# Kernel optimization log

Measured on AMD Instinct MI355X. Metric: run time of the kernel, lower is better.

## Reference

```python
import jax, jax.numpy as jnp
import numpy as np

B, D, N, K, T = 8192, 256, 2048, 512, 8
M_MARGIN = 1.0
LAMBDA_ORTHO = 1e-3
EPS = 1e-10


def _l2(a, b):
    # squared L2 distance along last axis
    return jnp.sum((a - b) ** 2, axis=-1)


def setup_inputs() -> dict:
    key = jax.random.key(0)
    k1, k2, k3, k4, k5 = jax.random.split(key, 5)
    return {
        "v": jax.random.normal(k1, (B, D), dtype=jnp.float32),
        "vhat": jax.random.normal(k2, (B, D), dtype=jnp.float32),
        "g": jax.random.uniform(k3, (B, K), dtype=jnp.float32),
        "F": jax.random.normal(k4, (K, D), dtype=jnp.float32),
        "negatives": jax.random.normal(k5, (N, D), dtype=jnp.float32),
        "mask": jnp.ones((B,), dtype=bool),
    }


def reference(v, vhat, g, F, negatives, mask):
    maskf = mask.astype(v.dtype)
    msum = maskf.sum()

    # ---- contrastive loss (vectorized over the N-negatives loop) ----
    true_dist = _l2(vhat, v)                                   # [B]
    neg_dist = _l2(vhat[:, None, :], negatives[None, :, :])    # [B, N]
    per = jnp.maximum(1.0 + true_dist[:, None] - neg_dist, 0.0)
    ju_per = per.mean(axis=1) * maskf                          # [B]
    Ju = jnp.where(msum == 0, 0.0, ju_per.sum() / msum)

    # ---- focal triplet loss (topk smallest g, gather F rows) ----
    _, idx = jax.lax.top_k(-g, T)                              # [B, T] indices of t smallest
    g_tz = jnp.take_along_axis(g, idx, axis=1)                 # [B, T]
    F_t = F[idx]                                               # [B, T, D]
    g_t = g_tz / (g_tz.sum(axis=1, keepdims=True) + EPS)
    m_t = M_MARGIN * (1.0 - g_t) ** 2                          # [B, T]
    d_neg = _l2(vhat[:, None, :], F_t)                         # [B, T]
    cur = jnp.maximum(m_t + true_dist[:, None] - d_neg, 0.0)
    jt_per = cur.sum(axis=1) * maskf
    Jt = jnp.where(msum == 0, 0.0, jt_per.sum() / msum)

    # ---- orthogonality regularizer: ||F F^T - I||_F, then squared ----
    gram = F @ F.T - jnp.eye(K, dtype=F.dtype)
    ortho = jnp.sqrt(jnp.sum(gram ** 2))

    Jz = Ju + Jt + LAMBDA_ORTHO * ortho ** 2
    return Jz
```

## Files before the change

### kernel.cpp

```cpp
#include <hip/hip_runtime.h>

#define B_N 8192
#define D_N 256
#define N_N 2048
#define K_N 512
#define T_N 8

using short8  = __attribute__((ext_vector_type(8))) short;
using floatx4 = __attribute__((ext_vector_type(4))) float;


__device__ __forceinline__ float wave_reduce_sum(float x) {
  #pragma unroll
  for (int off = 32; off > 0; off >>= 1) x += __shfl_down(x, off, 64);
  return x;
}

__device__ __forceinline__ unsigned int f2bf(float x) {
  unsigned u = __float_as_uint(x);
  return (u + 0x7fffu + ((u >> 16) & 1u)) >> 16;
}

__device__ __forceinline__ unsigned int pack2bf(float x, float y) {
  return f2bf(x) | (f2bf(y) << 16);
}

__device__ __forceinline__ void gload16(const unsigned short* g, unsigned short* l) {
  __builtin_amdgcn_global_load_lds(
      (const __attribute__((address_space(1))) unsigned int*)g,
      (__attribute__((address_space(3))) unsigned int*)l, 16, 0, 0);
}

__global__ __launch_bounds__(256) void prep_kernel(
    const float* __restrict__ v, const float* __restrict__ vhat,
    const float* __restrict__ neg, const float* __restrict__ F,
    unsigned short* __restrict__ vhat_bf, unsigned short* __restrict__ neg_bf,
    unsigned short* __restrict__ F_bf,
    float* __restrict__ td, float* __restrict__ vn2, float* __restrict__ cb,
    float* __restrict__ nn2, float* __restrict__ fn2) {
  int lane = threadIdx.x & 63;
  int row = (blockIdx.x << 2) + (threadIdx.x >> 6);
  if (row < B_N) {
    const float4 a = *(const float4*)(vhat + (size_t)row * D_N + lane * 4);
    const float4 b = *(const float4*)(v + (size_t)row * D_N + lane * 4);
    float dx = a.x - b.x, dy = a.y - b.y, dz = a.z - b.z, dw = a.w - b.w;
    float t = dx * dx + dy * dy + dz * dz + dw * dw;
    float n = a.x * a.x + a.y * a.y + a.z * a.z + a.w * a.w;
    uint2 p;
    p.x = pack2bf(a.x, a.y);
    p.y = pack2bf(a.z, a.w);
    *(uint2*)(vhat_bf + (size_t)row * D_N + lane * 4) = p;
    t = wave_reduce_sum(t);
    n = wave_reduce_sum(n);
    if (lane == 0) {
      td[row] = t;
      vn2[row] = n;
      cb[row] = 1.0f + t - n;
    }
  } else if (row < B_N + N_N) {
    int r = row - B_N;
    const float4 a = *(const float4*)(neg + (size_t)r * D_N + lane * 4);
    float n = a.x * a.x + a.y * a.y + a.z * a.z + a.w * a.w;
    uint2 p;
    p.x = pack2bf(a.x, a.y);
    p.y = pack2bf(a.z, a.w);
    *(uint2*)(neg_bf + (size_t)r * D_N + lane * 4) = p;
    n = wave_reduce_sum(n);
    if (lane == 0) nn2[r] = n;
  } else {
    int r = row - (B_N + N_N);
    const float4 a = *(const float4*)(F + (size_t)r * D_N + lane * 4);
    float n = a.x * a.x + a.y * a.y + a.z * a.z + a.w * a.w;
    uint2 p;
    p.x = pack2bf(a.x, a.y);
    p.y = pack2bf(a.z, a.w);
    *(uint2*)(F_bf + (size_t)r * D_N + lane * 4) = p;
    n = wave_reduce_sum(n);
    if (lane == 0) fn2[r] = n;
  }
}

__global__ __launch_bounds__(256) void main_kernel(
    const unsigned short* __restrict__ vhat_bf, const unsigned short* __restrict__ neg_bf,
    const unsigned short* __restrict__ F_bf,
    const float* __restrict__ g, const float* __restrict__ F,
    const float* __restrict__ vhat_f,
    const float* __restrict__ td, const float* __restrict__ vn2,
    const float* __restrict__ cb, const float* __restrict__ nn2,
    const float* __restrict__ fn2, const int* __restrict__ mask,
    float* __restrict__ ju_part, float* __restrict__ jt_row,
    float* __restrict__ or_part) {
  __shared__ __align__(16) unsigned char smem[16384];
  const int bx = blockIdx.x;
  const int tid = threadIdx.x;
  const int lane = tid & 63;
  const int wave = tid >> 6;

  if (bx < 1040) {
    const bool is_ju = bx < 1024;
    unsigned short* AsU = (unsigned short*)smem;
    unsigned short* BsU = AsU + 4096;
    int r0, c0;
    const unsigned short *Abase, *Bbase;
    if (is_ju) {
      r0 = (bx >> 4) * 128;
      c0 = (bx & 15) * 128;
      Abase = vhat_bf;
      Bbase = neg_bf;
    } else {
      int o = bx - 1024;
      r0 = (o >> 2) * 128;
      c0 = (o & 3) * 128;
      Abase = F_bf;
      Bbase = F_bf;
    }
    const int wx = wave & 1, wy = wave >> 1;

    const int c_slot = lane & 3;
    const int rA0 = wave * 32 + (lane >> 2);
    const int rA1 = rA0 + 16;
    const int cg0 = c_slot ^ ((rA0 >> 1) & 3);
    const int cg1 = c_slot ^ ((rA1 >> 1) & 3);
    const unsigned short* gA0 = Abase + (size_t)(r0 + rA0) * D_N + cg0 * 8;
    const unsigned short* gA1 = Abase + (size_t)(r0 + rA1) * D_N + cg1 * 8;
    const unsigned short* gB0 = Bbase + (size_t)(c0 + rA0) * D_N + cg0 * 8;
    const unsigned short* gB1 = Bbase + (size_t)(c0 + rA1) * D_N + cg1 * 8;
    unsigned short* lA0 = AsU + wave * 1024 + lane * 8;
    unsigned short* lA1 = lA0 + 512;
    unsigned short* lB0 = BsU + wave * 1024 + lane * 8;
    unsigned short* lB1 = lB0 + 512;

    const int fr = lane & 15;
    const int fc = lane >> 4;
    int aoff[4], boff[4];
    #pragma unroll
    for (int i = 0; i < 4; ++i) {
      int ra = wy * 64 + i * 16 + fr;
      aoff[i] = ra * 32 + (fc ^ ((ra >> 1) & 3)) * 8;
      int rb = wx * 64 + i * 16 + fr;
      boff[i] = rb * 32 + (fc ^ ((rb >> 1) & 3)) * 8;
    }

    floatx4 acc[4][4];
    #pragma unroll
    for (int i = 0; i < 4; ++i)
      #pragma unroll
      for (int j = 0; j < 4; ++j)
        acc[i][j] = floatx4{0.0f, 0.0f, 0.0f, 0.0f};

    for (int k0 = 0; k0 < D_N; k0 += 32) {
      __syncthreads();
      gload16(gA0 + k0, lA0);
      gload16(gA1 + k0, lA1);
      gload16(gB0 + k0, lB0);
      gload16(gB1 + k0, lB1);
      __syncthreads();
      short8 af[4], bf[4];
      #pragma unroll
      for (int i = 0; i < 4; ++i) af[i] = *(const short8*)(AsU + aoff[i]);
      #pragma unroll
      for (int j = 0; j < 4; ++j) bf[j] = *(const short8*)(BsU + boff[j]);
      #pragma unroll
      for (int i = 0; i < 4; ++i)
        #pragma unroll
        for (int j = 0; j < 4; ++j)
          acc[i][j] = __builtin_amdgcn_mfma_f32_16x16x32_bf16(af[i], bf[j], acc[i][j], 0, 0, 0);
    }

    if (is_ju) {
      float nns[4];
      #pragma unroll
      for (int j = 0; j < 4; ++j)
        nns[j] = nn2[c0 + wx * 64 + j * 16 + (lane & 15)];
      float lsum = 0.0f;
      #pragma unroll
      for (int i = 0; i < 4; ++i) {
        #pragma unroll
        for (int r = 0; r < 4; ++r) {
          int b = r0 + wy * 64 + i * 16 + (lane >> 4) * 4 + r;
          float cbb = cb[b];
          float mf = (mask[b] != 0) ? 1.0f : 0.0f;
          float rs = 0.0f;
          #pragma unroll
          for (int j = 0; j < 4; ++j) {
            float val = cbb + 2.0f * acc[i][j][r] - nns[j];
            rs += fmaxf(val, 0.0f);
          }
          lsum += mf * rs;
        }
      }
      lsum = wave_reduce_sum(lsum);
      if (lane == 0) ju_part[bx * 4 + wave] = lsum;
    } else {
      float lsum = 0.0f;
      #pragma unroll
      for (int i = 0; i < 4; ++i) {
        #pragma unroll
        for (int r = 0; r < 4; ++r) {
          int gi = r0 + wy * 64 + i * 16 + (lane >> 4) * 4 + r;
          #pragma unroll
          for (int j = 0; j < 4; ++j) {
            int gj = c0 + wx * 64 + j * 16 + (lane & 15);
            float s = (gi == gj) ? (fn2[gi] - 1.0f) : acc[i][j][r];
            lsum += s * s;
          }
        }
      }
      lsum = wave_reduce_sum(lsum);
      if (lane == 0) or_part[(bx - 1024) * 4 + wave] = lsum;
    }

  } else {
    int b = ((bx - 1040) << 2) + wave;
    const float* grow = g + (size_t)b * K_N;
    float gv[8];
    {
      float4 g0 = *(const float4*)(grow + lane * 8);
      float4 g1 = *(const float4*)(grow + lane * 8 + 4);
      gv[0] = g0.x; gv[1] = g0.y; gv[2] = g0.z; gv[3] = g0.w;
      gv[4] = g1.x; gv[5] = g1.y; gv[6] = g1.z; gv[7] = g1.w;
    }
    unsigned used = 0;
    float sel_val[T_N];
    int sel_idx[T_N];
    for (int t = 0; t < T_N; ++t) {
      float lv = 3.0e38f;
      int lj = 0;
      #pragma unroll
      for (int j = 0; j < 8; ++j) {
        bool ok = (((used >> j) & 1u) == 0u) && (gv[j] < lv);
        lv = ok ? gv[j] : lv;
        lj = ok ? j : lj;
      }
      float rv = lv;
      int ri = lane * 8 + lj;
      #pragma unroll
      for (int off = 32; off > 0; off >>= 1) {
        float ov = __shfl_down(rv, off, 64);
        int oi = __shfl_down(ri, off, 64);
        if (ov < rv) { rv = ov; ri = oi; }
      }
      rv = __shfl(rv, 0, 64);
      ri = __shfl(ri, 0, 64);
      if ((ri >> 3) == lane) used |= 1u << (ri & 7);
      sel_val[t] = rv;
      sel_idx[t] = ri;
    }
    float gsum = 1e-10f;
    #pragma unroll
    for (int t = 0; t < T_N; ++t) gsum += sel_val[t];
    float4 vh = *(const float4*)(vhat_f + (size_t)b * D_N + lane * 4);
    float tdb = td[b], vnb = vn2[b];
    float jtb = 0.0f;
    #pragma unroll
    for (int t = 0; t < T_N; ++t) {
      const float* Fr = F + (size_t)sel_idx[t] * D_N;
      float4 f4 = *(const float4*)(Fr + lane * 4);
      float p = vh.x * f4.x + vh.y * f4.y + vh.z * f4.z + vh.w * f4.w;
      p = wave_reduce_sum(p);
      p = __shfl(p, 0, 64);
      float dneg = vnb - 2.0f * p + fn2[sel_idx[t]];
      float gt = sel_val[t] / gsum;
      float mt = (1.0f - gt) * (1.0f - gt);
      float cur = mt + tdb - dneg;
      jtb += cur > 0.0f ? cur : 0.0f;
    }
    if (lane == 0) jt_row[b] = jtb * ((mask[b] != 0) ? 1.0f : 0.0f);
  }
}

__global__ __launch_bounds__(256) void finalize_kernel(
    const float* __restrict__ jt_row, const float* __restrict__ ju_part,
    const float* __restrict__ or_part, const int* __restrict__ mask,
    float* __restrict__ out) {
  int tid = threadIdx.x;
  float sjt = 0.0f, sju = 0.0f, sor = 0.0f, sm = 0.0f;
  for (int i = tid; i < B_N; i += 256) {
    sjt += jt_row[i];
    sm += (mask[i] != 0) ? 1.0f : 0.0f;
  }
  for (int i = tid; i < 4096; i += 256) sju += ju_part[i];
  if (tid < 64) sor = or_part[tid];
  sjt = wave_reduce_sum(sjt);
  sju = wave_reduce_sum(sju);
  sor = wave_reduce_sum(sor);
  sm  = wave_reduce_sum(sm);
  __shared__ float red[4][4];
  int lane = tid & 63, w = tid >> 6;
  if (lane == 0) {
    red[w][0] = sjt; red[w][1] = sju; red[w][2] = sor; red[w][3] = sm;
  }
  __syncthreads();
  if (tid == 0) {
    float jt = red[0][0] + red[1][0] + red[2][0] + red[3][0];
    float ju = red[0][1] + red[1][1] + red[2][1] + red[3][1];
    float oo = red[0][2] + red[1][2] + red[2][2] + red[3][2];
    float ms = red[0][3] + red[1][3] + red[2][3] + red[3][3];
    float Ju = (ms == 0.0f) ? 0.0f : ju / ((float)N_N * ms);
    float Jt = (ms == 0.0f) ? 0.0f : jt / ms;
    out[0] = Ju + Jt + 1.0e-3f * oo;
  }
}

extern "C" void kernel_launch(void* const* d_in, const int* in_sizes, int n_in,
                              void* d_out, int out_size, void* d_ws, size_t ws_size,
                              hipStream_t stream) {
  (void)in_sizes; (void)n_in; (void)out_size; (void)ws_size;
  const float* v    = (const float*)d_in[0];
  const float* vhat = (const float*)d_in[1];
  const float* g    = (const float*)d_in[2];
  const float* F    = (const float*)d_in[3];
  const float* neg  = (const float*)d_in[4];
  const int*   mask = (const int*)d_in[5];

  float* ws = (float*)d_ws;
  float* td      = ws;
  float* vn2     = ws + 8192;
  float* cb      = ws + 16384;
  float* nn2     = ws + 24576;
  float* fn2     = ws + 26624;
  float* jt_row  = ws + 27136;
  float* ju_part = ws + 35328;
  float* or_part = ws + 39424;
  unsigned short* vhat_bf = (unsigned short*)(ws + 39680);
  unsigned short* neg_bf  = vhat_bf + (size_t)B_N * D_N;
  unsigned short* F_bf    = neg_bf + (size_t)N_N * D_N;

  prep_kernel<<<(B_N + N_N + K_N) / 4, 256, 0, stream>>>(
      v, vhat, neg, F, vhat_bf, neg_bf, F_bf, td, vn2, cb, nn2, fn2);
  main_kernel<<<1024 + 16 + 2048, 256, 0, stream>>>(
      vhat_bf, neg_bf, F_bf, g, F, vhat, td, vn2, cb, nn2, fn2, mask,
      ju_part, jt_row, or_part);
  finalize_kernel<<<1, 256, 0, stream>>>(jt_row, ju_part, or_part, mask, (float*)d_out);
}
```

Baseline: 127.8 us.

## Compute triplet dot products via dense vhat·F^T MFMA GEMM and bitonic top-k

```diff
diff --git a/kernel.cpp b/kernel.cpp
--- a/kernel.cpp
+++ b/kernel.cpp
@@ -31,13 +31,26 @@
       (__attribute__((address_space(3))) unsigned int*)l, 16, 0, 0);
 }
 
+#define CSWAP(a, b)                                              \
+  {                                                              \
+    bool sw_ = sv[a] > sv[b];                                    \
+    float tv_ = sw_ ? sv[a] : sv[b];                             \
+    sv[a] = sw_ ? sv[b] : sv[a];                                 \
+    sv[b] = tv_;                                                 \
+    int ti_ = sw_ ? si[a] : si[b];                               \
+    si[a] = sw_ ? si[b] : si[a];                                 \
+    si[b] = ti_;                                                 \
+  }
+
 __global__ __launch_bounds__(256) void prep_kernel(
     const float* __restrict__ v, const float* __restrict__ vhat,
     const float* __restrict__ neg, const float* __restrict__ F,
+    const float* __restrict__ g,
     unsigned short* __restrict__ vhat_bf, unsigned short* __restrict__ neg_bf,
     unsigned short* __restrict__ F_bf,
     float* __restrict__ td, float* __restrict__ vn2, float* __restrict__ cb,
-    float* __restrict__ nn2, float* __restrict__ fn2) {
+    float* __restrict__ nn2, float* __restrict__ fn2,
+    float* __restrict__ selc, int* __restrict__ seli) {
   int lane = threadIdx.x & 63;
   int row = (blockIdx.x << 2) + (threadIdx.x >> 6);
   if (row < B_N) {
@@ -56,6 +69,60 @@
       td[row] = t;
       vn2[row] = n;
       cb[row] = 1.0f + t - n;
+    }
+    const float* grow = g + (size_t)row * K_N;
+    float sv[8];
+    int si[8];
+    {
+      float4 g0 = *(const float4*)(grow + lane * 8);
+      float4 g1 = *(const float4*)(grow + lane * 8 + 4);
+      sv[0] = g0.x; sv[1] = g0.y; sv[2] = g0.z; sv[3] = g0.w;
+      sv[4] = g1.x; sv[5] = g1.y; sv[6] = g1.z; sv[7] = g1.w;
+      #pragma unroll
+      for (int j = 0; j < 8; ++j) si[j] = lane * 8 + j;
+    }
+    CSWAP(0,1) CSWAP(2,3) CSWAP(4,5) CSWAP(6,7)
+    CSWAP(0,2) CSWAP(1,3) CSWAP(4,6) CSWAP(5,7)
+    CSWAP(1,2) CSWAP(5,6)
+    CSWAP(0,4) CSWAP(1,5) CSWAP(2,6) CSWAP(3,7)
+    CSWAP(2,4) CSWAP(3,5)
+    CSWAP(1,2) CSWAP(3,4) CSWAP(5,6)
+    #pragma unroll
+    for (int rr = 0; rr < 6; ++rr) {
+      const int msk = 1 << rr;
+      float pv[8];
+      int pi[8];
+      #pragma unroll
+      for (int j = 0; j < 8; ++j) {
+        pv[j] = __shfl_xor(sv[j], msk, 64);
+        pi[j] = __shfl_xor(si[j], msk, 64);
+      }
+      float cv[8];
+      int ci[8];
+      #pragma unroll
+      for (int j = 0; j < 8; ++j) {
+        bool mine = sv[j] <= pv[7 - j];
+        cv[j] = mine ? sv[j] : pv[7 - j];
+        ci[j] = mine ? si[j] : pi[7 - j];
+      }
+      #pragma unroll
+      for (int j = 0; j < 8; ++j) { sv[j] = cv[j]; si[j] = ci[j]; }
+      CSWAP(0,4) CSWAP(1,5) CSWAP(2,6) CSWAP(3,7)
+      CSWAP(0,2) CSWAP(1,3) CSWAP(4,6) CSWAP(5,7)
+      CSWAP(0,1) CSWAP(2,3) CSWAP(4,5) CSWAP(6,7)
+    }
+    float gsum = 1e-10f;
+    #pragma unroll
+    for (int t8 = 0; t8 < T_N; ++t8) gsum += sv[t8];
+    if (lane == 0) {
+      float base = t - n;
+      #pragma unroll
+      for (int t8 = 0; t8 < T_N; ++t8) {
+        float gt = sv[t8] / gsum;
+        float mt = (1.0f - gt) * (1.0f - gt);
+        selc[(size_t)row * T_N + t8] = mt + base;
+        seli[(size_t)row * T_N + t8] = si[t8];
+      }
     }
   } else if (row < B_N + N_N) {
     int r = row - B_N;
@@ -83,204 +150,190 @@
 __global__ __launch_bounds__(256) void main_kernel(
     const unsigned short* __restrict__ vhat_bf, const unsigned short* __restrict__ neg_bf,
     const unsigned short* __restrict__ F_bf,
-    const float* __restrict__ g, const float* __restrict__ F,
-    const float* __restrict__ vhat_f,
-    const float* __restrict__ td, const float* __restrict__ vn2,
     const float* __restrict__ cb, const float* __restrict__ nn2,
     const float* __restrict__ fn2, const int* __restrict__ mask,
-    float* __restrict__ ju_part, float* __restrict__ jt_row,
-    float* __restrict__ or_part) {
+    float* __restrict__ ju_part, float* __restrict__ or_part,
+    float* __restrict__ W) {
   __shared__ __align__(16) unsigned char smem[16384];
   const int bx = blockIdx.x;
   const int tid = threadIdx.x;
   const int lane = tid & 63;
   const int wave = tid >> 6;
 
-  if (bx < 1040) {
-    const bool is_ju = bx < 1024;
-    unsigned short* AsU = (unsigned short*)smem;
-    unsigned short* BsU = AsU + 4096;
-    int r0, c0;
-    const unsigned short *Abase, *Bbase;
-    if (is_ju) {
-      r0 = (bx >> 4) * 128;
-      c0 = (bx & 15) * 128;
-      Abase = vhat_bf;
-      Bbase = neg_bf;
-    } else {
-      int o = bx - 1024;
-      r0 = (o >> 2) * 128;
-      c0 = (o & 3) * 128;
-      Abase = F_bf;
-      Bbase = F_bf;
-    }
-    const int wx = wave & 1, wy = wave >> 1;
-
-    const int c_slot = lane & 3;
-    const int rA0 = wave * 32 + (lane >> 2);
-    const int rA1 = rA0 + 16;
-    const int cg0 = c_slot ^ ((rA0 >> 1) & 3);
-    const int cg1 = c_slot ^ ((rA1 >> 1) & 3);
-    const unsigned short* gA0 = Abase + (size_t)(r0 + rA0) * D_N + cg0 * 8;
-    const unsigned short* gA1 = Abase + (size_t)(r0 + rA1) * D_N + cg1 * 8;
-    const unsigned short* gB0 = Bbase + (size_t)(c0 + rA0) * D_N + cg0 * 8;
-    const unsigned short* gB1 = Bbase + (size_t)(c0 + rA1) * D_N + cg1 * 8;
-    unsigned short* lA0 = AsU + wave * 1024 + lane * 8;
-    unsigned short* lA1 = lA0 + 512;
-    unsigned short* lB0 = BsU + wave * 1024 + lane * 8;
-    unsigned short* lB1 = lB0 + 512;
-
-    const int fr = lane & 15;
-    const int fc = lane >> 4;
-    int aoff[4], boff[4];
+  unsigned short* AsU = (unsigned short*)smem;
+  unsigned short* BsU = AsU + 4096;
+  int r0, c0;
+  const unsigned short *Abase, *Bbase;
+  int seg;
+  if (bx < 1024) {
+    seg = 0;
+    r0 = (bx >> 4) * 128;
+    c0 = (bx & 15) * 128;
+    Abase = vhat_bf;
+    Bbase = neg_bf;
+  } else if (bx < 1040) {
+    seg = 1;
+    int o = bx - 1024;
+    r0 = (o >> 2) * 128;
+    c0 = (o & 3) * 128;
+    Abase = F_bf;
+    Bbase = F_bf;
+  } else {
+    seg = 2;
+    int o = bx - 1040;
+    r0 = (o >> 2) * 128;
+    c0 = (o & 3) * 128;
+    Abase = vhat_bf;
+    Bbase = F_bf;
+  }
+  const int wx = wave & 1, wy = wave >> 1;
+
+  const int c_slot = lane & 3;
+  const int rA0 = wave * 32 + (lane >> 2);
+  const int rA1 = rA0 + 16;
+  const int cg0 = c_slot ^ ((rA0 >> 1) & 3);
+  const int cg1 = c_slot ^ ((rA1 >> 1) & 3);
+  const unsigned short* gA0 = Abase + (size_t)(r0 + rA0) * D_N + cg0 * 8;
+  const unsigned short* gA1 = Abase + (size_t)(r0 + rA1) * D_N + cg1 * 8;
+  const unsigned short* gB0 = Bbase + (size_t)(c0 + rA0) * D_N + cg0 * 8;
+  const unsigned short* gB1 = Bbase + (size_t)(c0 + rA1) * D_N + cg1 * 8;
+  unsigned short* lA0 = AsU + wave * 1024 + lane * 8;
+  unsigned short* lA1 = lA0 + 512;
+  unsigned short* lB0 = BsU + wave * 1024 + lane * 8;
+  unsigned short* lB1 = lB0 + 512;
+
+  const int fr = lane & 15;
+  const int fc = lane >> 4;
+  int aoff[4], boff[4];
+  #pragma unroll
+  for (int i = 0; i < 4; ++i) {
+    int ra = wy * 64 + i * 16 + fr;
+    aoff[i] = ra * 32 + (fc ^ ((ra >> 1) & 3)) * 8;
+    int rb = wx * 64 + i * 16 + fr;
+    boff[i] = rb * 32 + (fc ^ ((rb >> 1) & 3)) * 8;
+  }
+
+  floatx4 acc[4][4];
+  #pragma unroll
+  for (int i = 0; i < 4; ++i)
+    #pragma unroll
+    for (int j = 0; j < 4; ++j)
+      acc[i][j] = floatx4{0.0f, 0.0f, 0.0f, 0.0f};
+
+  for (int k0 = 0; k0 < D_N; k0 += 32) {
+    __syncthreads();
+    gload16(gA0 + k0, lA0);
+    gload16(gA1 + k0, lA1);
+    gload16(gB0 + k0, lB0);
+    gload16(gB1 + k0, lB1);
+    __syncthreads();
+    short8 af[4], bf[4];
+    #pragma unroll
+    for (int i = 0; i < 4; ++i) af[i] = *(const short8*)(AsU + aoff[i]);
+    #pragma unroll
+    for (int j = 0; j < 4; ++j) bf[j] = *(const short8*)(BsU + boff[j]);
+    #pragma unroll
+    for (int i = 0; i < 4; ++i)
+      #pragma unroll
+      for (int j = 0; j < 4; ++j)
+        acc[i][j] = __builtin_amdgcn_mfma_f32_16x16x32_bf16(af[i], bf[j], acc[i][j], 0, 0, 0);
+  }
+
+  if (seg == 0) {
+    float nns[4];
+    #pragma unroll
+    for (int j = 0; j < 4; ++j)
+      nns[j] = nn2[c0 + wx * 64 + j * 16 + (lane & 15)];
+    float lsum = 0.0f;
     #pragma unroll
     for (int i = 0; i < 4; ++i) {
-      int ra = wy * 64 + i * 16 + fr;
-      aoff[i] = ra * 32 + (fc ^ ((ra >> 1) & 3)) * 8;
-      int rb = wx * 64 + i * 16 + fr;
-      boff[i] = rb * 32 + (fc ^ ((rb >> 1) & 3)) * 8;
-    }
-
-    floatx4 acc[4][4];
-    #pragma unroll
-    for (int i = 0; i < 4; ++i)
-      #pragma unroll
-      for (int j = 0; j < 4; ++j)
-        acc[i][j] = floatx4{0.0f, 0.0f, 0.0f, 0.0f};
-
-    for (int k0 = 0; k0 < D_N; k0 += 32) {
-      __syncthreads();
-      gload16(gA0 + k0, lA0);
-      gload16(gA1 + k0, lA1);
-      gload16(gB0 + k0, lB0);
-      gload16(gB1 + k0, lB1);
-      __syncthreads();
-      short8 af[4], bf[4];
-      #pragma unroll
-      for (int i = 0; i < 4; ++i) af[i] = *(const short8*)(AsU + aoff[i]);
-      #pragma unroll
-      for (int j = 0; j < 4; ++j) bf[j] = *(const short8*)(BsU + boff[j]);
-      #pragma unroll
-      for (int i = 0; i < 4; ++i)
+      #pragma unroll
+      for (int r = 0; r < 4; ++r) {
+        int b = r0 + wy * 64 + i * 16 + (lane >> 4) * 4 + r;
+        float cbb = cb[b];
+        float mf = (mask[b] != 0) ? 1.0f : 0.0f;
+        float rs = 0.0f;
         #pragma unroll
-        for (int j = 0; j < 4; ++j)
-          acc[i][j] = __builtin_amdgcn_mfma_f32_16x16x32_bf16(af[i], bf[j], acc[i][j], 0, 0, 0);
-    }
-
-    if (is_ju) {
-      float nns[4];
-      #pragma unroll
-      for (int j = 0; j < 4; ++j)
-        nns[j] = nn2[c0 + wx * 64 + j * 16 + (lane & 15)];
-      float lsum = 0.0f;
-      #pragma unroll
-      for (int i = 0; i < 4; ++i) {
+        for (int j = 0; j < 4; ++j) {
+          float val = cbb + 2.0f * acc[i][j][r] - nns[j];
+          rs += fmaxf(val, 0.0f);
+        }
+        lsum += mf * rs;
+      }
+    }
+    lsum = wave_reduce_sum(lsum);
+    if (lane == 0) ju_part[bx * 4 + wave] = lsum;
+  } else if (seg == 1) {
+    float lsum = 0.0f;
+    #pragma unroll
+    for (int i = 0; i < 4; ++i) {
+      #pragma unroll
+      for (int r = 0; r < 4; ++r) {
+        int gi = r0 + wy * 64 + i * 16 + (lane >> 4) * 4 + r;
         #pragma unroll
-        for (int r = 0; r < 4; ++r) {
-          int b = r0 + wy * 64 + i * 16 + (lane >> 4) * 4 + r;
-          float cbb = cb[b];
-          float mf = (mask[b] != 0) ? 1.0f : 0.0f;
-          float rs = 0.0f;
-          #pragma unroll
-          for (int j = 0; j < 4; ++j) {
-            float val = cbb + 2.0f * acc[i][j][r] - nns[j];
-            rs += fmaxf(val, 0.0f);
-          }
-          lsum += mf * rs;
+        for (int j = 0; j < 4; ++j) {
+          int gj = c0 + wx * 64 + j * 16 + (lane & 15);
+          float s = (gi == gj) ? (fn2[gi] - 1.0f) : acc[i][j][r];
+          lsum += s * s;
         }
       }
-      lsum = wave_reduce_sum(lsum);
-      if (lane == 0) ju_part[bx * 4 + wave] = lsum;
-    } else {
-      float lsum = 0.0f;
-      #pragma unroll
-      for (int i = 0; i < 4; ++i) {
+    }
+    lsum = wave_reduce_sum(lsum);
+    if (lane == 0) or_part[(bx - 1024) * 4 + wave] = lsum;
+  } else {
+    #pragma unroll
+    for (int i = 0; i < 4; ++i) {
+      #pragma unroll
+      for (int r = 0; r < 4; ++r) {
+        int row = r0 + wy * 64 + i * 16 + (lane >> 4) * 4 + r;
         #pragma unroll
-        for (int r = 0; r < 4; ++r) {
-          int gi = r0 + wy * 64 + i * 16 + (lane >> 4) * 4 + r;
-          #pragma unroll
-          for (int j = 0; j < 4; ++j) {
-            int gj = c0 + wx * 64 + j * 16 + (lane & 15);
-            float s = (gi == gj) ? (fn2[gi] - 1.0f) : acc[i][j][r];
-            lsum += s * s;
-          }
+        for (int j = 0; j < 4; ++j) {
+          int col = c0 + wx * 64 + j * 16 + (lane & 15);
+          W[(size_t)row * K_N + col] = acc[i][j][r];
         }
       }
-      lsum = wave_reduce_sum(lsum);
-      if (lane == 0) or_part[(bx - 1024) * 4 + wave] = lsum;
-    }
-
-  } else {
-    int b = ((bx - 1040) << 2) + wave;
-    const float* grow = g + (size_t)b * K_N;
-    float gv[8];
-    {
-      float4 g0 = *(const float4*)(grow + lane * 8);
-      float4 g1 = *(const float4*)(grow + lane * 8 + 4);
-      gv[0] = g0.x; gv[1] = g0.y; gv[2] = g0.z; gv[3] = g0.w;
-      gv[4] = g1.x; gv[5] = g1.y; gv[6] = g1.z; gv[7] = g1.w;
-    }
-    unsigned used = 0;
-    float sel_val[T_N];
-    int sel_idx[T_N];
-    for (int t = 0; t < T_N; ++t) {
-      float lv = 3.0e38f;
-      int lj = 0;
-      #pragma unroll
-      for (int j = 0; j < 8; ++j) {
-        bool ok = (((used >> j) & 1u) == 0u) && (gv[j] < lv);
-        lv = ok ? gv[j] : lv;
-        lj = ok ? j : lj;
-      }
-      float rv = lv;
-      int ri = lane * 8 + lj;
-      #pragma unroll
-      for (int off = 32; off > 0; off >>= 1) {
-        float ov = __shfl_down(rv, off, 64);
-        int oi = __shfl_down(ri, off, 64);
-        if (ov < rv) { rv = ov; ri = oi; }
-      }
-      rv = __shfl(rv, 0, 64);
-      ri = __shfl(ri, 0, 64);
-      if ((ri >> 3) == lane) used |= 1u << (ri & 7);
-      sel_val[t] = rv;
-      sel_idx[t] = ri;
-    }
-    float gsum = 1e-10f;
-    #pragma unroll
-    for (int t = 0; t < T_N; ++t) gsum += sel_val[t];
-    float4 vh = *(const float4*)(vhat_f + (size_t)b * D_N + lane * 4);
-    float tdb = td[b], vnb = vn2[b];
-    float jtb = 0.0f;
-    #pragma unroll
-    for (int t = 0; t < T_N; ++t) {
-      const float* Fr = F + (size_t)sel_idx[t] * D_N;
-      float4 f4 = *(const float4*)(Fr + lane * 4);
-      float p = vh.x * f4.x + vh.y * f4.y + vh.z * f4.z + vh.w * f4.w;
-      p = wave_reduce_sum(p);
-      p = __shfl(p, 0, 64);
-      float dneg = vnb - 2.0f * p + fn2[sel_idx[t]];
-      float gt = sel_val[t] / gsum;
-      float mt = (1.0f - gt) * (1.0f - gt);
-      float cur = mt + tdb - dneg;
-      jtb += cur > 0.0f ? cur : 0.0f;
-    }
-    if (lane == 0) jt_row[b] = jtb * ((mask[b] != 0) ? 1.0f : 0.0f);
-  }
+    }
+  }
+}
+
+__global__ __launch_bounds__(256) void jt_gather_kernel(
+    const int* __restrict__ seli, const float* __restrict__ selc,
+    const float* __restrict__ W, const float* __restrict__ fn2,
+    const int* __restrict__ mask, float* __restrict__ jt_part) {
+  int b = blockIdx.x * 256 + threadIdx.x;
+  int4 i0 = *(const int4*)(seli + (size_t)b * 8);
+  int4 i1 = *(const int4*)(seli + (size_t)b * 8 + 4);
+  float4 c0 = *(const float4*)(selc + (size_t)b * 8);
+  float4 c1 = *(const float4*)(selc + (size_t)b * 8 + 4);
+  const float* wrow = W + (size_t)b * K_N;
+  float s = 0.0f;
+  s += fmaxf(c0.x + 2.0f * wrow[i0.x] - fn2[i0.x], 0.0f);
+  s += fmaxf(c0.y + 2.0f * wrow[i0.y] - fn2[i0.y], 0.0f);
+  s += fmaxf(c0.z + 2.0f * wrow[i0.z] - fn2[i0.z], 0.0f);
+  s += fmaxf(c0.w + 2.0f * wrow[i0.w] - fn2[i0.w], 0.0f);
+  s += fmaxf(c1.x + 2.0f * wrow[i1.x] - fn2[i1.x], 0.0f);
+  s += fmaxf(c1.y + 2.0f * wrow[i1.y] - fn2[i1.y], 0.0f);
+  s += fmaxf(c1.z + 2.0f * wrow[i1.z] - fn2[i1.z], 0.0f);
+  s += fmaxf(c1.w + 2.0f * wrow[i1.w] - fn2[i1.w], 0.0f);
+  s *= (mask[b] != 0) ? 1.0f : 0.0f;
+  s = wave_reduce_sum(s);
+  __shared__ float red[4];
+  if ((threadIdx.x & 63) == 0) red[threadIdx.x >> 6] = s;
+  __syncthreads();
+  if (threadIdx.x == 0)
+    jt_part[blockIdx.x] = red[0] + red[1] + red[2] + red[3];
 }
 
 __global__ __launch_bounds__(256) void finalize_kernel(
-    const float* __restrict__ jt_row, const float* __restrict__ ju_part,
+    const float* __restrict__ jt_part, const float* __restrict__ ju_part,
     const float* __restrict__ or_part, const int* __restrict__ mask,
     float* __restrict__ out) {
   int tid = threadIdx.x;
   float sjt = 0.0f, sju = 0.0f, sor = 0.0f, sm = 0.0f;
-  for (int i = tid; i < B_N; i += 256) {
-    sjt += jt_row[i];
-    sm += (mask[i] != 0) ? 1.0f : 0.0f;
-  }
+  for (int i = tid; i < B_N; i += 256) sm += (mask[i] != 0) ? 1.0f : 0.0f;
   for (int i = tid; i < 4096; i += 256) sju += ju_part[i];
   if (tid < 64) sor = or_part[tid];
+  if (tid < 32) sjt = jt_part[tid];
   sjt = wave_reduce_sum(sjt);
   sju = wave_reduce_sum(sju);
   sor = wave_reduce_sum(sor);
@@ -314,22 +367,28 @@
   const int*   mask = (const int*)d_in[5];
 
   float* ws = (float*)d_ws;
-  float* td      = ws;
-  float* vn2     = ws + 8192;
-  float* cb      = ws + 16384;
-  float* nn2     = ws + 24576;
-  float* fn2     = ws + 26624;
-  float* jt_row  = ws + 27136;
-  float* ju_part = ws + 35328;
-  float* or_part = ws + 39424;
-  unsigned short* vhat_bf = (unsigned short*)(ws + 39680);
+  float* W       = ws;
+  float* td      = ws + 4194304;
+  float* vn2     = ws + 4202496;
+  float* cb      = ws + 4210688;
+  float* nn2     = ws + 4218880;
+  float* fn2     = ws + 4220928;
+  float* ju_part = ws + 4221440;
+  float* or_part = ws + 4225536;
+  float* jt_part = ws + 4225600;
+  float* selc    = ws + 4225632;
+  int*   seli    = (int*)(ws + 4291168);
+  unsigned short* vhat_bf = (unsigned short*)(ws + 4356704);
   unsigned short* neg_bf  = vhat_bf + (size_t)B_N * D_N;
   unsigned short* F_bf    = neg_bf + (size_t)N_N * D_N;
 
   prep_kernel<<<(B_N + N_N + K_N) / 4, 256, 0, stream>>>(
-      v, vhat, neg, F, vhat_bf, neg_bf, F_bf, td, vn2, cb, nn2, fn2);
-  main_kernel<<<1024 + 16 + 2048, 256, 0, stream>>>(
-      vhat_bf, neg_bf, F_bf, g, F, vhat, td, vn2, cb, nn2, fn2, mask,
-      ju_part, jt_row, or_part);
-  finalize_kernel<<<1, 256, 0, stream>>>(jt_row, ju_part, or_part, mask, (float*)d_out);
-}
+      v, vhat, neg, F, g, vhat_bf, neg_bf, F_bf, td, vn2, cb, nn2, fn2,
+      selc, seli);
+  main_kernel<<<1024 + 16 + 256, 256, 0, stream>>>(
+      vhat_bf, neg_bf, F_bf, cb, nn2, fn2, mask, ju_part, or_part, W);
+  jt_gather_kernel<<<B_N / 256, 256, 0, stream>>>(
+      seli, selc, W, fn2, mask, jt_part);
+  finalize_kernel<<<1, 256, 0, stream>>>(jt_part, ju_part, or_part, mask,
+                                         (float*)d_out);
+}
```

Result: no change. 126.3 us (-1.2%).
